# Performance work log

Measured on AMD Instinct MI355X. Metric: run time of the kernel, lower is better.

Reference implementation:

```python
import jax, jax.numpy as jnp
import numpy as np

DIM = 192
RES = 64
NUM_HEADS = 4
H_SP, W_SP = RES, 4  # idx == 0
SCALE = (DIM // NUM_HEADS) ** (-0.5)


def conv2d(x, w, b, pad, groups=1):
    y = jax.lax.conv_general_dilated(
        x, w, window_strides=(1, 1), padding=[(pad, pad), (pad, pad)],
        dimension_numbers=("NCHW", "OIHW", "NCHW"), feature_group_count=groups)
    return y + b[None, :, None, None]


def img2windows(img, H_sp, W_sp):
    B, C, H, W = img.shape
    x = img.reshape(B, C, H // H_sp, H_sp, W // W_sp, W_sp)
    return jnp.transpose(x, (0, 2, 4, 3, 5, 1)).reshape(-1, H_sp * W_sp, C)


def windows2img(w, H_sp, W_sp, H, W):
    Bw = w.shape[0]
    B = Bw // ((H // H_sp) * (W // W_sp))
    x = w.reshape(B, H // H_sp, W // W_sp, H_sp, W_sp, -1)
    return jnp.transpose(x, (0, 5, 1, 3, 2, 4)).reshape(B, -1, H, W)


def im2cswin(x):
    w = img2windows(x, H_SP, W_SP)  # [B', L, C]
    Bw, L, C = w.shape
    return jnp.transpose(w.reshape(Bw, L, NUM_HEADS, C // NUM_HEADS), (0, 2, 1, 3))


def setup_inputs() -> dict:
    key = jax.random.key(0)
    ks = jax.random.split(key, 11)
    s = 0.02
    return {
        "x": jax.random.normal(ks[0], (32, DIM, RES, RES), jnp.float32),
        "w_qk": jax.random.normal(ks[1], (2 * DIM, DIM, 1, 1), jnp.float32) * s,
        "b_qk": jnp.zeros((2 * DIM,), jnp.float32),
        "w_q5": jax.random.normal(ks[2], (DIM, 1, 5, 5), jnp.float32) * s,
        "b_q5": jnp.zeros((DIM,), jnp.float32),
        "w_k5": jax.random.normal(ks[3], (DIM, 1, 5, 5), jnp.float32) * s,
        "b_k5": jnp.zeros((DIM,), jnp.float32),
        "w_v": jax.random.normal(ks[4], (DIM, DIM, 1, 1), jnp.float32) * s,
        "b_v": jnp.zeros((DIM,), jnp.float32),
        "w_cape": jax.random.normal(ks[5], (DIM, 1, 5, 5), jnp.float32) * s,
        "b_cape": jnp.zeros((DIM,), jnp.float32),
    }


def reference(x, w_qk, b_qk, w_q5, b_q5, w_k5, b_k5, w_v, b_v, w_cape, b_cape):
    B, C, H, W = x.shape
    qk = conv2d(x, w_qk, b_qk, pad=0)
    q, k = jnp.split(qk, 2, axis=1)
    v = conv2d(x, w_v, b_v, pad=0)
    cape = conv2d(v, w_cape, b_cape, pad=2, groups=DIM)  # depthwise 5x5
    q = im2cswin(conv2d(q, w_q5, b_q5, pad=2, groups=DIM) + cape)
    k = im2cswin(conv2d(k, w_k5, b_k5, pad=2, groups=DIM) + cape)
    vw = im2cswin(v)
    q = q * SCALE
    attn = jnp.einsum("whqd,whkd->whqk", q, k)  # windows, heads, L, L
    attn = jax.nn.softmax(attn, axis=-1)
    out = jnp.einsum("whqk,whkd->whqd", attn, vw)
    Bw = out.shape[0]
    out = jnp.transpose(out, (0, 2, 1, 3)).reshape(Bw, H_SP * W_SP, C)
    return windows2img(out, H_SP, W_SP, H, W) + cape
```

## Files before the change

### kernel.cpp

```cpp
#include <hip/hip_runtime.h>

typedef short short8 __attribute__((ext_vector_type(8)));
typedef float f32x4 __attribute__((ext_vector_type(4)));

#define BATCH 32
#define DIM 192
#define RES 64
#define HW 4096
#define NH 4
#define DH 48
#define NWIN 16
#define LTOK 256
#define BUFE (BATCH * DIM * HW)
#define SCALE_Q 0.14433756729740643f

__device__ __forceinline__ unsigned short f2bf(float f) {
  unsigned int u = __builtin_bit_cast(unsigned int, f);
  u += 0x7fffu + ((u >> 16) & 1u);
  return (unsigned short)(u >> 16);
}
__device__ __forceinline__ float bf2f(unsigned short h) {
  unsigned int u = ((unsigned int)h) << 16;
  return __builtin_bit_cast(float, u);
}
__device__ __forceinline__ f32x4 mfma16(short8 a, short8 b, f32x4 c) {
  return __builtin_amdgcn_mfma_f32_16x16x32_bf16(a, b, c, 0, 0, 0);
}

__global__ __launch_bounds__(256) void k0_wcvt(
    const float* __restrict__ w_qk, const float* __restrict__ w_v,
    unsigned short* __restrict__ wbf) {
  int u = blockIdx.x * 256 + threadIdx.x;
  int i4 = u * 4;
  const float* src = (i4 < 2 * DIM * DIM) ? (w_qk + i4) : (w_v + (i4 - 2 * DIM * DIM));
  float4 f = *(const float4*)src;
  uint2 pk;
  pk.x = (unsigned int)f2bf(f.x) | ((unsigned int)f2bf(f.y) << 16);
  pk.y = (unsigned int)f2bf(f.z) | ((unsigned int)f2bf(f.w) << 16);
  *(uint2*)&wbf[i4] = pk;
}

__global__ __launch_bounds__(256, 2) void k1_conv1x1(
    const float* __restrict__ x, const unsigned short* __restrict__ wbf,
    const float* __restrict__ b_qk, const float* __restrict__ b_v,
    unsigned short* __restrict__ q_raw, unsigned short* __restrict__ k_raw,
    unsigned short* __restrict__ v_buf) {
  __shared__ unsigned short Al[96 * 200];
  __shared__ unsigned short Bl[64 * 200];
  __shared__ unsigned short Os[96 * 68];
  const int tid = threadIdx.x;
  const int pix0 = blockIdx.x * 64;
  const int b = blockIdx.y;

  {
    const float* xb = x + (size_t)b * (DIM * HW) + pix0;
    int px = tid & 63;
    int icq = tid >> 6;
    for (int it = 0; it < 6; ++it) {
      int ic8 = icq + it * 4;
      const float* p = xb + (size_t)(ic8 * 8) * HW + px;
      unsigned short h[8];
#pragma unroll
      for (int j = 0; j < 8; ++j) h[j] = f2bf(p[(size_t)j * HW]);
      uint4 pk;
      pk.x = h[0] | ((unsigned int)h[1] << 16);
      pk.y = h[2] | ((unsigned int)h[3] << 16);
      pk.z = h[4] | ((unsigned int)h[5] << 16);
      pk.w = h[6] | ((unsigned int)h[7] << 16);
      *(uint4*)&Bl[px * 200 + ic8 * 8] = pk;
    }
  }

  const int lane = tid & 63, wv = tid >> 6;
  const int quad = lane >> 4, col = lane & 15;
  const int m0 = (wv >> 1) * 48, n0 = (wv & 1) * 32;
  const int wrow = tid / 24, wpart = tid % 24;

  for (int t = 0; t < 6; ++t) {
    {
      const unsigned short* wsrc = wbf + t * (96 * 192);
      uint4 tmp[9];
#pragma unroll
      for (int it = 0; it < 9; ++it) {
        int row = (it * 256 + tid) / 24, part = (it * 256 + tid) % 24;
        tmp[it] = *(const uint4*)(wsrc + row * 192 + part * 8);
      }
#pragma unroll
      for (int it = 0; it < 9; ++it) {
        int row = (it * 256 + tid) / 24, part = (it * 256 + tid) % 24;
        *(uint4*)&Al[row * 200 + part * 8] = tmp[it];
      }
      (void)wrow; (void)wpart;
    }
    __syncthreads();

    f32x4 acc[3][2];
#pragma unroll
    for (int fm = 0; fm < 3; ++fm)
#pragma unroll
      for (int fn = 0; fn < 2; ++fn) {
        acc[fm][fn][0] = 0.f; acc[fm][fn][1] = 0.f;
        acc[fm][fn][2] = 0.f; acc[fm][fn][3] = 0.f;
      }

#pragma unroll
    for (int ks = 0; ks < 6; ++ks) {
      short8 a[3], bb[2];
#pragma unroll
      for (int fm = 0; fm < 3; ++fm)
        a[fm] = *(const short8*)&Al[(m0 + fm * 16 + col) * 200 + ks * 32 + quad * 8];
#pragma unroll
      for (int fn = 0; fn < 2; ++fn)
        bb[fn] = *(const short8*)&Bl[(n0 + fn * 16 + col) * 200 + ks * 32 + quad * 8];
#pragma unroll
      for (int fm = 0; fm < 3; ++fm)
#pragma unroll
        for (int fn = 0; fn < 2; ++fn) acc[fm][fn] = mfma16(a[fm], bb[fn], acc[fm][fn]);
    }

    const int oc0 = t * 96;
#pragma unroll
    for (int fm = 0; fm < 3; ++fm) {
#pragma unroll
      for (int r = 0; r < 4; ++r) {
        int ocoff = m0 + fm * 16 + quad * 4 + r;
        int ocg = oc0 + ocoff;
        float bias = (ocg < 384) ? b_qk[ocg] : b_v[ocg - 384];
#pragma unroll
        for (int fn = 0; fn < 2; ++fn) {
          int px = n0 + fn * 16 + col;
          Os[ocoff * 68 + px] = f2bf(acc[fm][fn][r] + bias);
        }
      }
    }
    __syncthreads();

    unsigned short* dst;
    int ocbase;
    if (oc0 < 192) { dst = q_raw; ocbase = oc0; }
    else if (oc0 < 384) { dst = k_raw; ocbase = oc0 - 192; }
    else { dst = v_buf; ocbase = oc0 - 384; }
    {
      int row0 = tid >> 3, part = tid & 7;
#pragma unroll
      for (int it = 0; it < 3; ++it) {
        int row = it * 32 + row0;
        *(uint4*)&dst[((size_t)b * DIM + (ocbase + row)) * HW + pix0 + part * 8] =
            *(const uint4*)&Os[row * 68 + part * 8];
      }
    }
  }
}

__global__ __launch_bounds__(256) void k2_cape(
    const unsigned short* __restrict__ v_buf, const float* __restrict__ w_cape,
    const float* __restrict__ b_cape, float* __restrict__ cape_out) {
  const int c = blockIdx.y, b = blockIdx.z;
  const int h = blockIdx.x * 16 + (threadIdx.x >> 4);
  const int w4 = threadIdx.x & 15;
  const unsigned short* vp = v_buf + ((size_t)b * DIM + c) * HW;
  float wk[25];
#pragma unroll
  for (int i = 0; i < 25; ++i) wk[i] = w_cape[c * 25 + i];
  float acc[4];
  float bz = b_cape[c];
  acc[0] = acc[1] = acc[2] = acc[3] = bz;
#pragma unroll
  for (int dy = 0; dy < 5; ++dy) {
    int hr = h + dy - 2;
    float row[8];
    if (hr >= 0 && hr < RES) {
      const unsigned short* rp = vp + hr * RES + w4 * 4 - 2;
#pragma unroll
      for (int j = 0; j < 4; ++j) {
        int wc = w4 * 4 - 2 + 2 * j;
        unsigned int d = (wc >= 0 && wc < RES) ? *(const unsigned int*)(rp + 2 * j) : 0u;
        row[2 * j] = bf2f((unsigned short)(d & 0xffff));
        row[2 * j + 1] = bf2f((unsigned short)(d >> 16));
      }
    } else {
#pragma unroll
      for (int j = 0; j < 8; ++j) row[j] = 0.f;
    }
#pragma unroll
    for (int wj = 0; wj < 4; ++wj)
#pragma unroll
      for (int dx = 0; dx < 5; ++dx) acc[wj] += row[wj + dx] * wk[dy * 5 + dx];
  }
  float4 o;
  o.x = acc[0]; o.y = acc[1]; o.z = acc[2]; o.w = acc[3];
  *(float4*)&cape_out[((size_t)b * DIM + c) * HW + h * RES + w4 * 4] = o;
}

__global__ __launch_bounds__(256) void k3_dw(
    const unsigned short* __restrict__ src, const float* __restrict__ w5,
    const float* __restrict__ b5, const float* __restrict__ cape,
    unsigned short* __restrict__ dst_w, float scale) {
  __shared__ unsigned short patch[64 * 168];
  __shared__ unsigned short outS[64 * 72];
  const int lid = blockIdx.x;
  const int xx = lid & 7;
  const int ii = lid >> 3;
  const int b = xx * 4 + ii / 192;
  const int rem = ii % 192;
  const int wb = rem / 12;
  const int rr2 = rem % 12;
  const int ct = rr2 >> 2, ht = rr2 & 3;
  const int c0 = ct * 64, h0 = ht * 16;
  const int tid = threadIdx.x;

  for (int it = 0; it < 5; ++it) {
    int u = it * 256 + tid;
    int c = u / 20, rr = u % 20;
    int hr = h0 - 2 + rr;
    uint4 pk;
    pk.x = pk.y = pk.z = pk.w = 0u;
    if (hr >= 0 && hr < RES) {
      const unsigned short* rp =
          src + ((size_t)b * DIM + c0 + c) * HW + hr * RES + wb * 4 - 2;
      unsigned int dw[4];
#pragma unroll
      for (int j = 0; j < 4; ++j) {
        int wc = wb * 4 - 2 + 2 * j;
        dw[j] = (wc >= 0 && wc < RES) ? *(const unsigned int*)(rp + 2 * j) : 0u;
      }
      pk.x = dw[0]; pk.y = dw[1]; pk.z = dw[2]; pk.w = dw[3];
    }
    *(uint4*)&patch[c * 168 + rr * 8] = pk;
  }
  __syncthreads();

  const int c = tid >> 2, hq = tid & 3;
  float wk[25];
#pragma unroll
  for (int i = 0; i < 25; ++i) wk[i] = w5[(c0 + c) * 25 + i];
  float bz = b5[c0 + c];
  float acc[4][4];
#pragma unroll
  for (int j = 0; j < 4; ++j)
#pragma unroll
    for (int wm = 0; wm < 4; ++wm) acc[j][wm] = bz;

#pragma unroll
  for (int rel = 0; rel < 8; ++rel) {
    int p = hq * 4 + rel;
    uint4 pk = *(const uint4*)&patch[c * 168 + p * 8];
    float f8[8];
    f8[0] = bf2f((unsigned short)(pk.x & 0xffff));
    f8[1] = bf2f((unsigned short)(pk.x >> 16));
    f8[2] = bf2f((unsigned short)(pk.y & 0xffff));
    f8[3] = bf2f((unsigned short)(pk.y >> 16));
    f8[4] = bf2f((unsigned short)(pk.z & 0xffff));
    f8[5] = bf2f((unsigned short)(pk.z >> 16));
    f8[6] = bf2f((unsigned short)(pk.w & 0xffff));
    f8[7] = bf2f((unsigned short)(pk.w >> 16));
#pragma unroll
    for (int j = 0; j < 4; ++j) {
      int dy = rel - j;
      if (dy >= 0 && dy <= 4) {
#pragma unroll
        for (int wm = 0; wm < 4; ++wm)
#pragma unroll
          for (int dx = 0; dx < 5; ++dx) acc[j][wm] += f8[wm + dx] * wk[dy * 5 + dx];
      }
    }
  }

  size_t cpbase = ((size_t)b * DIM + c0 + c) * HW + (size_t)wb * 4;
#pragma unroll
  for (int j = 0; j < 4; ++j) {
    int h = h0 + hq * 4 + j;
    float4 cp = *(const float4*)&cape[cpbase + (size_t)h * RES];
    int lb = (hq * 4 + j) * 4;
    outS[(lb + 0) * 72 + c] = f2bf((acc[j][0] + cp.x) * scale);
    outS[(lb + 1) * 72 + c] = f2bf((acc[j][1] + cp.y) * scale);
    outS[(lb + 2) * 72 + c] = f2bf((acc[j][2] + cp.z) * scale);
    outS[(lb + 3) * 72 + c] = f2bf((acc[j][3] + cp.w) * scale);
  }
  __syncthreads();

  const size_t obase = ((size_t)(b * NWIN + wb) * LTOK + (size_t)h0 * 4) * DIM + c0;
  for (int it = 0; it < 2; ++it) {
    int u = it * 256 + tid;
    int ll = u >> 3, part = u & 7;
    *(uint4*)&dst_w[obase + (size_t)ll * DIM + part * 8] =
        *(const uint4*)&outS[ll * 72 + part * 8];
  }
}

#define KSTR 56
#define VSTR 256
#define PSTR 264

__global__ __launch_bounds__(256, 2) void k5_attn(
    const unsigned short* __restrict__ qf_w, const unsigned short* __restrict__ kf_w,
    const unsigned short* __restrict__ v_buf, unsigned short* __restrict__ out_w) {
  __shared__ unsigned short smem[29184];
  unsigned short* Kl = smem;
  unsigned short* Pl = smem;
  unsigned short* Vl = smem + 16896;

  const int lid = blockIdx.x;
  const int xx = lid & 7;
  const int ii = lid >> 3;
  const int b = (xx << 2) | (ii >> 8);
  const int rem = ii & 255;
  const int wb = rem >> 4;
  const int hd = (rem >> 2) & 3;
  const int qt = rem & 3;
  const int wi = b * NWIN + wb;

  const int tid = threadIdx.x, lane = tid & 63, wv = tid >> 6;
  const int quad = lane >> 4, col = lane & 15;
  const int q = qt * 64 + wv * 16 + col;

  const unsigned short* qp = qf_w + ((size_t)wi * LTOK + q) * DIM + hd * DH;
  short8 z8 = {0, 0, 0, 0, 0, 0, 0, 0};
  short8 bq0 = *(const short8*)(qp + quad * 8);
  short8 bq1 = z8;
  if (quad < 2) bq1 = *(const short8*)(qp + 32 + quad * 8);

  {
    const unsigned short* ks = kf_w + (size_t)wi * LTOK * DIM + hd * DH;
    for (int it = 0; it < 6; ++it) {
      int u = it * 256 + tid;
      int kl = u / 6, part = u % 6;
      *(uint4*)&Kl[kl * KSTR + part * 8] = *(const uint4*)(ks + (size_t)kl * DIM + part * 8);
    }
  }
  {
    const unsigned short* vs = v_buf + ((size_t)b * DIM + hd * DH) * HW + wb * 4;
    for (int it = 0; it < 12; ++it) {
      int u = it * 256 + tid;
      int d = u >> 6, h = u & 63;
      int kl8 = h >> 1;
      int off = ((kl8 ^ (d & 7)) * 8) + (h & 1) * 4;
      *(uint2*)&Vl[d * VSTR + off] = *(const uint2*)(vs + (size_t)d * HW + h * RES);
    }
  }
  __syncthreads();

  f32x4 s[16];
#pragma unroll
  for (int i = 0; i < 16; ++i) { s[i][0] = 0.f; s[i][1] = 0.f; s[i][2] = 0.f; s[i][3] = 0.f; }
#pragma unroll
  for (int fm = 0; fm < 16; ++fm) {
    short8 a0 = *(const short8*)&Kl[(fm * 16 + col) * KSTR + quad * 8];
    s[fm] = mfma16(a0, bq0, s[fm]);
  }
#pragma unroll
  for (int fm = 0; fm < 16; ++fm) {
    short8 a1 = z8;
    if (quad < 2) a1 = *(const short8*)&Kl[(fm * 16 + col) * KSTR + 32 + quad * 8];
    s[fm] = mfma16(a1, bq1, s[fm]);
  }

  float mx = s[0][0];
#pragma unroll
  for (int fm = 0; fm < 16; ++fm)
#pragma unroll
    for (int r = 0; r < 4; ++r) mx = fmaxf(mx, s[fm][r]);
  mx = fmaxf(mx, __shfl_xor(mx, 16));
  mx = fmaxf(mx, __shfl_xor(mx, 32));
  float sm = 0.f;
#pragma unroll
  for (int fm = 0; fm < 16; ++fm)
#pragma unroll
    for (int r = 0; r < 4; ++r) {
      float e = __expf(s[fm][r] - mx);
      s[fm][r] = e;
      sm += e;
    }
  sm += __shfl_xor(sm, 16);
  sm += __shfl_xor(sm, 32);
  float inv = 1.f / sm;

  __syncthreads();

  {
    unsigned short* Pw = Pl + (wv * 16 + col) * PSTR;
#pragma unroll
    for (int fm = 0; fm < 16; ++fm) {
      uint2 pk;
      pk.x = (unsigned int)f2bf(s[fm][0] * inv) | ((unsigned int)f2bf(s[fm][1] * inv) << 16);
      pk.y = (unsigned int)f2bf(s[fm][2] * inv) | ((unsigned int)f2bf(s[fm][3] * inv) << 16);
      *(uint2*)&Pw[fm * 16 + quad * 4] = pk;
    }
  }

  f32x4 o[3];
#pragma unroll
  for (int i = 0; i < 3; ++i) { o[i][0] = 0.f; o[i][1] = 0.f; o[i][2] = 0.f; o[i][3] = 0.f; }
#pragma unroll
  for (int ksi = 0; ksi < 8; ++ksi) {
    short8 a = *(const short8*)&Pl[(wv * 16 + col) * PSTR + ksi * 32 + quad * 8];
#pragma unroll
    for (int fn = 0; fn < 3; ++fn) {
      int d = fn * 16 + col;
      short8 bb = *(const short8*)&Vl[d * VSTR + (((ksi * 4 + quad) ^ (d & 7)) * 8)];
      o[fn] = mfma16(a, bb, o[fn]);
    }
  }

  {
    unsigned short* dst = out_w + ((size_t)wi * LTOK + qt * 64 + wv * 16) * DIM + hd * DH;
#pragma unroll
    for (int fn = 0; fn < 3; ++fn)
#pragma unroll
      for (int r = 0; r < 4; ++r)
        dst[(size_t)(quad * 4 + r) * DIM + fn * 16 + col] = f2bf(o[fn][r]);
  }
}

__global__ __launch_bounds__(256) void k6_final(
    const unsigned short* __restrict__ out_w, float* __restrict__ io) {
  __shared__ float tile[16 * 528];
  const int ht = blockIdx.x, ct = blockIdx.y, b = blockIdx.z;
  const int c0 = ct * 16, h0 = ht * 8;
  const int tid = threadIdx.x;
  for (int it = 0; it < 4; ++it) {
    int u = it * 256 + tid;
    int chunk = u & 1, l5 = (u >> 1) & 31, wb = u >> 6;
    const unsigned short* p =
        out_w + ((size_t)(b * NWIN + wb) * LTOK + (size_t)(h0 * 4 + l5)) * DIM + c0 + chunk * 8;
    uint4 pk = *(const uint4*)p;
    int h = l5 >> 2, wm = l5 & 3;
    float* t = &tile[(chunk * 8) * 528 + h * 66 + wb * 4 + wm];
    t[0 * 528] = bf2f((unsigned short)(pk.x & 0xffff));
    t[1 * 528] = bf2f((unsigned short)(pk.x >> 16));
    t[2 * 528] = bf2f((unsigned short)(pk.y & 0xffff));
    t[3 * 528] = bf2f((unsigned short)(pk.y >> 16));
    t[4 * 528] = bf2f((unsigned short)(pk.z & 0xffff));
    t[5 * 528] = bf2f((unsigned short)(pk.z >> 16));
    t[6 * 528] = bf2f((unsigned short)(pk.w & 0xffff));
    t[7 * 528] = bf2f((unsigned short)(pk.w >> 16));
  }
  __syncthreads();
  for (int it = 0; it < 8; ++it) {
    int u = it * 256 + tid;
    int w16 = u & 15, h = (u >> 4) & 7, c = u >> 7;
    size_t g = ((size_t)b * DIM + c0 + c) * HW + (size_t)(h0 + h) * RES + w16 * 4;
    float4 cp = *(const float4*)&io[g];
    float4 ov;
    ov.x = tile[c * 528 + h * 66 + w16 * 4 + 0] + cp.x;
    ov.y = tile[c * 528 + h * 66 + w16 * 4 + 1] + cp.y;
    ov.z = tile[c * 528 + h * 66 + w16 * 4 + 2] + cp.z;
    ov.w = tile[c * 528 + h * 66 + w16 * 4 + 3] + cp.w;
    *(float4*)&io[g] = ov;
  }
}

extern "C" void kernel_launch(void* const* d_in, const int* in_sizes, int n_in,
                              void* d_out, int out_size, void* d_ws, size_t ws_size,
                              hipStream_t stream) {
  (void)in_sizes; (void)n_in; (void)out_size; (void)ws_size;
  const float* x = (const float*)d_in[0];
  const float* w_qk = (const float*)d_in[1];
  const float* b_qk = (const float*)d_in[2];
  const float* w_q5 = (const float*)d_in[3];
  const float* b_q5 = (const float*)d_in[4];
  const float* w_k5 = (const float*)d_in[5];
  const float* b_k5 = (const float*)d_in[6];
  const float* w_v = (const float*)d_in[7];
  const float* b_v = (const float*)d_in[8];
  const float* w_cape = (const float*)d_in[9];
  const float* b_cape = (const float*)d_in[10];
  float* out = (float*)d_out;

  unsigned short* ws = (unsigned short*)d_ws;
  unsigned short* buf0 = ws;
  unsigned short* buf1 = ws + (size_t)BUFE;
  unsigned short* buf2 = ws + (size_t)BUFE * 2;
  unsigned short* buf3 = ws + (size_t)BUFE * 3;

  k0_wcvt<<<dim3(108), 256, 0, stream>>>(w_qk, w_v, buf3);
  k1_conv1x1<<<dim3(64, 32), 256, 0, stream>>>(x, buf3, b_qk, b_v, buf0, buf1, buf2);
  k2_cape<<<dim3(4, 192, 32), 256, 0, stream>>>(buf2, w_cape, b_cape, out);
  k3_dw<<<dim3(6144), 256, 0, stream>>>(buf0, w_q5, b_q5, out, buf3, SCALE_Q);
  k3_dw<<<dim3(6144), 256, 0, stream>>>(buf1, w_k5, b_k5, out, buf0, 1.0f);
  k5_attn<<<dim3(8192), 256, 0, stream>>>(buf3, buf0, buf2, buf1);
  k6_final<<<dim3(8, 12, 32), 256, 0, stream>>>(buf1, out);
}
```

Baseline: 705.9 us.

## Redistribute softmax probabilities via ds_bpermute instead of LDS round-trip in attention

```diff
diff --git a/kernel.cpp b/kernel.cpp
--- a/kernel.cpp
+++ b/kernel.cpp
@@ -2,6 +2,7 @@
 
 typedef short short8 __attribute__((ext_vector_type(8)));
 typedef float f32x4 __attribute__((ext_vector_type(4)));
+typedef int i32x4 __attribute__((ext_vector_type(4)));
 
 #define BATCH 32
 #define DIM 192
@@ -74,7 +75,6 @@
   const int lane = tid & 63, wv = tid >> 6;
   const int quad = lane >> 4, col = lane & 15;
   const int m0 = (wv >> 1) * 48, n0 = (wv & 1) * 32;
-  const int wrow = tid / 24, wpart = tid % 24;
 
   for (int t = 0; t < 6; ++t) {
     {
@@ -90,7 +90,6 @@
         int row = (it * 256 + tid) / 24, part = (it * 256 + tid) % 24;
         *(uint4*)&Al[row * 200 + part * 8] = tmp[it];
       }
-      (void)wrow; (void)wpart;
     }
     __syncthreads();
 
@@ -290,15 +289,13 @@
 
 #define KSTR 56
 #define VSTR 256
-#define PSTR 264
-
-__global__ __launch_bounds__(256, 2) void k5_attn(
+
+__global__ __launch_bounds__(256, 3) void k5_attn(
     const unsigned short* __restrict__ qf_w, const unsigned short* __restrict__ kf_w,
     const unsigned short* __restrict__ v_buf, unsigned short* __restrict__ out_w) {
-  __shared__ unsigned short smem[29184];
+  __shared__ unsigned short smem[26624];
   unsigned short* Kl = smem;
-  unsigned short* Pl = smem;
-  unsigned short* Vl = smem + 16896;
+  unsigned short* Vl = smem + 14336;
 
   const int lid = blockIdx.x;
   const int xx = lid & 7;
@@ -375,25 +372,37 @@
   sm += __shfl_xor(sm, 32);
   float inv = 1.f / sm;
 
-  __syncthreads();
-
-  {
-    unsigned short* Pw = Pl + (wv * 16 + col) * PSTR;
-#pragma unroll
-    for (int fm = 0; fm < 16; ++fm) {
-      uint2 pk;
-      pk.x = (unsigned int)f2bf(s[fm][0] * inv) | ((unsigned int)f2bf(s[fm][1] * inv) << 16);
-      pk.y = (unsigned int)f2bf(s[fm][2] * inv) | ((unsigned int)f2bf(s[fm][3] * inv) << 16);
-      *(uint2*)&Pw[fm * 16 + quad * 4] = pk;
-    }
-  }
+  unsigned int w0[16], w1[16];
+#pragma unroll
+  for (int fm = 0; fm < 16; ++fm) {
+    w0[fm] = (unsigned int)f2bf(s[fm][0] * inv) | ((unsigned int)f2bf(s[fm][1] * inv) << 16);
+    w1[fm] = (unsigned int)f2bf(s[fm][2] * inv) | ((unsigned int)f2bf(s[fm][3] * inv) << 16);
+  }
+
+  const int aA = (32 * (quad & 1) + col) * 4;
+  const int aB = aA + 64;
+  const bool lowq = quad < 2;
 
   f32x4 o[3];
 #pragma unroll
   for (int i = 0; i < 3; ++i) { o[i][0] = 0.f; o[i][1] = 0.f; o[i][2] = 0.f; o[i][3] = 0.f; }
 #pragma unroll
   for (int ksi = 0; ksi < 8; ++ksi) {
-    short8 a = *(const short8*)&Pl[(wv * 16 + col) * PSTR + ksi * 32 + quad * 8];
+    const int fe = 2 * ksi, fo = 2 * ksi + 1;
+    int e0 = __builtin_amdgcn_ds_bpermute(aA, (int)w0[fe]);
+    int g0 = __builtin_amdgcn_ds_bpermute(aA, (int)w0[fo]);
+    int e1 = __builtin_amdgcn_ds_bpermute(aA, (int)w1[fe]);
+    int g1 = __builtin_amdgcn_ds_bpermute(aA, (int)w1[fo]);
+    int e2 = __builtin_amdgcn_ds_bpermute(aB, (int)w0[fe]);
+    int g2 = __builtin_amdgcn_ds_bpermute(aB, (int)w0[fo]);
+    int e3 = __builtin_amdgcn_ds_bpermute(aB, (int)w1[fe]);
+    int g3 = __builtin_amdgcn_ds_bpermute(aB, (int)w1[fo]);
+    i32x4 aw;
+    aw[0] = lowq ? e0 : g0;
+    aw[1] = lowq ? e1 : g1;
+    aw[2] = lowq ? e2 : g2;
+    aw[3] = lowq ? e3 : g3;
+    short8 a = __builtin_bit_cast(short8, aw);
 #pragma unroll
     for (int fn = 0; fn < 3; ++fn) {
       int d = fn * 16 + col;
```

New measurement: 699.1 us. Within noise of the previous version (-1.0%).
